# Optimization experiments

Measured on AMD Instinct MI355X. Metric: run time of the kernel, lower is better.

## Reference

```python
import jax, jax.numpy as jnp
import numpy as np

HIDDEN = 1024
FFN = 2816
N_EXPERTS = 8
TOP_K = 2
EPS = 1e-5
B, S = 2, 2048


def setup_inputs() -> dict:
    key = jax.random.key(0)
    ks = jax.random.split(key, 5)
    scale = 0.02
    return {
        "hidden_states": jax.random.normal(ks[0], (B, S, HIDDEN), dtype=jnp.float32),
        "ln_weight": jnp.ones((HIDDEN,), dtype=jnp.float32),
        "router_w": jax.random.normal(ks[1], (HIDDEN, N_EXPERTS), dtype=jnp.float32) * scale,
        "w1": jax.random.normal(ks[2], (N_EXPERTS, HIDDEN, FFN), dtype=jnp.float32) * scale,
        "w3": jax.random.normal(ks[3], (N_EXPERTS, HIDDEN, FFN), dtype=jnp.float32) * scale,
        "w2": jax.random.normal(ks[4], (N_EXPERTS, FFN, HIDDEN), dtype=jnp.float32) * scale,
    }


def _rms_norm(x, weight, eps):
    # LlamaRMSNorm: fp32 variance, scale by weight
    var = jnp.mean(jnp.square(x), axis=-1, keepdims=True)
    return x * jax.lax.rsqrt(var + eps) * weight


def reference(hidden_states, ln_weight, router_w, w1, w3, w2):
    b, s, h = hidden_states.shape
    x = _rms_norm(hidden_states, ln_weight, EPS).reshape(b * s, h)  # [T,H]

    # TopKRouter: softmax over experts, keep top-k gate probs
    logits = x @ router_w                       # [T,E]
    probs = jax.nn.softmax(logits, axis=-1)     # [T,E]
    top_p, top_i = jax.lax.top_k(probs, TOP_K)  # [T,K]
    # sparse gate matrix [T,E]: prob where selected, else 0 (dispatch+combine weights)
    gates = jnp.sum(jax.nn.one_hot(top_i, N_EXPERTS, dtype=x.dtype) * top_p[..., None], axis=1)

    # Experts: gated MLP (SwiGLU) per expert; dense-dispatch reference form,
    # combine masks out non-routed (gate==0) contributions.
    h1 = jnp.einsum("td,edf->tef", x, w1)       # [T,E,F]
    h3 = jnp.einsum("td,edf->tef", x, w3)       # [T,E,F]
    act = jax.nn.silu(h1) * h3                  # [T,E,F]
    y = jnp.einsum("tef,efd->ted", act, w2)     # [T,E,H]

    out = jnp.einsum("te,ted->td", gates, y)    # combine: [T,H]
    return out.reshape(b, s, h)
```

## Files before the change

### kernel.cpp

```cpp
#include <hip/hip_runtime.h>
#include <cstdint>
#include <cstddef>

#define TOKS 4096
#define HID  1024
#define FFN  2816
#define NE   8
#define CAP  4096

using floatx4 = __attribute__((ext_vector_type(4))) float;
using bf16x8  = __attribute__((ext_vector_type(8))) short;

__device__ __forceinline__ unsigned short f2bf(float f) {
    union { float f; unsigned int u; } v; v.f = f;
    unsigned int r = v.u + 0x7FFFu + ((v.u >> 16) & 1u);
    return (unsigned short)(r >> 16);
}

#define GLOAD16(g, l) __builtin_amdgcn_global_load_lds( \
    (__attribute__((address_space(1))) void*)(g),        \
    (__attribute__((address_space(3))) void*)(l), 16, 0, 0)

__global__ __launch_bounds__(256) void k_rmsnorm(const float* __restrict__ x,
                                                 const float* __restrict__ g,
                                                 unsigned short* __restrict__ xn)
{
    const int t = blockIdx.x;
    const int tid = threadIdx.x;
    const float4 v = *(const float4*)(x + (size_t)t*HID + tid*4);
    float ss = v.x*v.x + v.y*v.y + v.z*v.z + v.w*v.w;
    #pragma unroll
    for (int s = 32; s; s >>= 1) ss += __shfl_xor(ss, s, 64);
    __shared__ float red[4];
    if ((tid & 63) == 0) red[tid >> 6] = ss;
    __syncthreads();
    const float tot = red[0] + red[1] + red[2] + red[3];
    const float sc = rsqrtf(tot * (1.0f/HID) + 1e-5f);
    const float4 gw = *(const float4*)(g + tid*4);
    ushort4 o;
    o.x = f2bf(v.x*sc*gw.x); o.y = f2bf(v.y*sc*gw.y);
    o.z = f2bf(v.z*sc*gw.z); o.w = f2bf(v.w*sc*gw.w);
    *(ushort4*)(xn + (size_t)t*HID + tid*4) = o;
}

__global__ __launch_bounds__(256) void k_router(const float* __restrict__ x,
                                                const float* __restrict__ g,
                                                const float* __restrict__ rw,
                                                int* __restrict__ cnt,
                                                int* __restrict__ ids,
                                                float* __restrict__ gates)
{
    const int wid = threadIdx.x >> 6, lane = threadIdx.x & 63;
    const int t = blockIdx.x*4 + wid;
    const float* xr = x + (size_t)t*HID;
    float ss = 0.f;
    float acc[NE];
    #pragma unroll
    for (int e = 0; e < NE; ++e) acc[e] = 0.f;
    for (int h = lane; h < HID; h += 64) {
        const float xv = xr[h];
        ss += xv*xv;
        const float xg = xv * g[h];
        const float4 r0 = *(const float4*)(rw + h*NE);
        const float4 r1 = *(const float4*)(rw + h*NE + 4);
        acc[0] += xg*r0.x; acc[1] += xg*r0.y; acc[2] += xg*r0.z; acc[3] += xg*r0.w;
        acc[4] += xg*r1.x; acc[5] += xg*r1.y; acc[6] += xg*r1.z; acc[7] += xg*r1.w;
    }
    #pragma unroll
    for (int s = 32; s; s >>= 1) {
        ss += __shfl_xor(ss, s, 64);
        #pragma unroll
        for (int e = 0; e < NE; ++e) acc[e] += __shfl_xor(acc[e], s, 64);
    }
    if (lane == 0) {
        const float sc = rsqrtf(ss * (1.0f/HID) + 1e-5f);
        float p[NE];
        float m = -1e30f;
        #pragma unroll
        for (int e = 0; e < NE; ++e) { p[e] = acc[e]*sc; if (p[e] > m) m = p[e]; }
        float sum = 0.f;
        #pragma unroll
        for (int e = 0; e < NE; ++e) { p[e] = __expf(p[e] - m); sum += p[e]; }
        const float inv = 1.f / sum;
        int i1 = 0; float p1 = p[0];
        #pragma unroll
        for (int e = 1; e < NE; ++e) if (p[e] > p1) { p1 = p[e]; i1 = e; }
        int i2 = -1; float p2 = -1.f;
        #pragma unroll
        for (int e = 0; e < NE; ++e) if (e != i1 && p[e] > p2) { p2 = p[e]; i2 = e; }
        int s0 = atomicAdd(cnt + i1, 1);
        ids[i1*CAP + s0] = t; gates[i1*CAP + s0] = p1*inv;
        int s1 = atomicAdd(cnt + i2, 1);
        ids[i2*CAP + s1] = t; gates[i2*CAP + s1] = p2*inv;
    }
}

__global__ void k_scan(const int* __restrict__ cnt, int* __restrict__ off)
{
    if (threadIdx.x == 0) {
        int s = 0;
        for (int e = 0; e < NE; ++e) { off[e] = s; s += cnt[e]; }
        off[NE] = s;
    }
}

__global__ __launch_bounds__(256) void k_convtrans(const float* __restrict__ w1,
                                                   const float* __restrict__ w3,
                                                   const float* __restrict__ w2,
                                                   unsigned short* __restrict__ w1t,
                                                   unsigned short* __restrict__ w3t,
                                                   unsigned short* __restrict__ w2t)
{
    const int which = blockIdx.y;
    const int e = blockIdx.z;
    const float* src; unsigned short* dst; int R, C;
    if (which == 0)      { src = w1; dst = w1t; R = HID; C = FFN; }
    else if (which == 1) { src = w3; dst = w3t; R = HID; C = FFN; }
    else                 { src = w2; dst = w2t; R = FFN; C = HID; }
    src += (size_t)e * R * C;
    dst += (size_t)e * R * C;
    const int tiles_r = R >> 6;
    const int tr = blockIdx.x % tiles_r;
    const int tc = blockIdx.x / tiles_r;
    const int r0 = tr << 6, c0 = tc << 6;
    __shared__ unsigned short lds[64*66];
    const int tid = threadIdx.x;
    #pragma unroll
    for (int it = 0; it < 4; ++it) {
        const int id = it*256 + tid;
        const int r = id >> 4;
        const int c4 = (id & 15) << 2;
        const float4 v = *(const float4*)(src + (size_t)(r0 + r)*C + c0 + c4);
        lds[r*66 + c4 + 0] = f2bf(v.x);
        lds[r*66 + c4 + 1] = f2bf(v.y);
        lds[r*66 + c4 + 2] = f2bf(v.z);
        lds[r*66 + c4 + 3] = f2bf(v.w);
    }
    __syncthreads();
    #pragma unroll
    for (int it = 0; it < 2; ++it) {
        const int id = it*256 + tid;
        const int cc = id >> 3;
        const int rv = (id & 7) << 3;
        bf16x8 o;
        #pragma unroll
        for (int j = 0; j < 8; ++j) o[j] = (short)lds[(rv + j)*66 + cc];
        *(bf16x8*)(dst + (size_t)(c0 + cc)*R + r0 + rv) = o;
    }
}

__global__ __launch_bounds__(256, 4) void k_gemm1(
    const unsigned short* __restrict__ xn,
    const unsigned short* __restrict__ w1t,
    const unsigned short* __restrict__ w3t,
    const int* __restrict__ ids,
    const int* __restrict__ cnt,
    const int* __restrict__ off,
    unsigned short* __restrict__ act)
{
    const int e = blockIdx.z;
    const int cn = cnt[e];
    const int m0 = blockIdx.y * 128;
    if (m0 >= cn) return;
    const int n0 = blockIdx.x * 64;
    const int base = off[e];

    __shared__ __align__(16) unsigned short sA [128*64];
    __shared__ __align__(16) unsigned short sB1[64*64];
    __shared__ __align__(16) unsigned short sB3[64*64];

    const int tid  = threadIdx.x;
    const int wid  = tid >> 6;
    const int lane = tid & 63;
    const int lrow = lane >> 3;
    const int lchk = lane & 7;

    const unsigned short* aG[4];
    #pragma unroll
    for (int j = 0; j < 4; ++j) {
        const int row = (wid*4 + j)*8 + lrow;
        int rr = m0 + row; if (rr > cn - 1) rr = cn - 1;
        const int tok = ids[e*CAP + rr];
        const int c = lchk ^ (row & 7);
        aG[j] = xn + (size_t)tok*HID + c*8;
    }
    const unsigned short *b1G[2], *b3G[2];
    #pragma unroll
    for (int j = 0; j < 2; ++j) {
        const int row = (wid*2 + j)*8 + lrow;
        const int n = n0 + row;
        const int c = lchk ^ (row & 7);
        b1G[j] = w1t + ((size_t)e*FFN + n)*HID + c*8;
        b3G[j] = w3t + ((size_t)e*FFN + n)*HID + c*8;
    }

    floatx4 acc1[4][2], acc3[4][2];
    #pragma unroll
    for (int a = 0; a < 4; ++a)
      #pragma unroll
      for (int b = 0; b < 2; ++b) {
        acc1[a][b] = (floatx4){0.f,0.f,0.f,0.f};
        acc3[a][b] = (floatx4){0.f,0.f,0.f,0.f};
      }

    const int wm  = (wid >> 1) * 64;
    const int wn  = (wid & 1) * 32;
    const int r16 = lane & 15;
    const int q   = lane >> 4;
    const int rsw = r16 & 7;

    for (int kt = 0; kt < HID; kt += 64) {
        __syncthreads();
        #pragma unroll
        for (int j = 0; j < 4; ++j) GLOAD16(aG[j] + kt, sA + (wid*4 + j)*512);
        #pragma unroll
        for (int j = 0; j < 2; ++j) {
            GLOAD16(b1G[j] + kt, sB1 + (wid*2 + j)*512);
            GLOAD16(b3G[j] + kt, sB3 + (wid*2 + j)*512);
        }
        __syncthreads();
        #pragma unroll
        for (int kk = 0; kk < 2; ++kk) {
            const int slot = ((kk*4 + q) ^ rsw) << 3;
            bf16x8 a[4];
            #pragma unroll
            for (int mt = 0; mt < 4; ++mt)
                a[mt] = *(const bf16x8*)(sA + (wm + mt*16 + r16)*64 + slot);
            #pragma unroll
            for (int nt = 0; nt < 2; ++nt) {
                const bf16x8 b1 = *(const bf16x8*)(sB1 + (wn + nt*16 + r16)*64 + slot);
                const bf16x8 b3 = *(const bf16x8*)(sB3 + (wn + nt*16 + r16)*64 + slot);
                #pragma unroll
                for (int mt = 0; mt < 4; ++mt) {
                    acc1[mt][nt] = __builtin_amdgcn_mfma_f32_16x16x32_bf16(a[mt], b1, acc1[mt][nt], 0, 0, 0);
                    acc3[mt][nt] = __builtin_amdgcn_mfma_f32_16x16x32_bf16(a[mt], b3, acc3[mt][nt], 0, 0, 0);
                }
            }
        }
    }

    #pragma unroll
    for (int mt = 0; mt < 4; ++mt)
      #pragma unroll
      for (int i = 0; i < 4; ++i) {
        const int row = wm + mt*16 + q*4 + i;
        if (m0 + row < cn) {
            unsigned short* rp = act + (size_t)(base + m0 + row)*FFN + n0 + wn + r16;
            #pragma unroll
            for (int nt = 0; nt < 2; ++nt) {
                const float h1 = acc1[mt][nt][i];
                const float h3 = acc3[mt][nt][i];
                rp[nt*16] = f2bf(h1 / (1.f + __expf(-h1)) * h3);
            }
        }
      }
}

__global__ __launch_bounds__(256, 4) void k_gemm2(
    const unsigned short* __restrict__ act,
    const unsigned short* __restrict__ w2t,
    const int* __restrict__ ids,
    const float* __restrict__ gates,
    const int* __restrict__ cnt,
    const int* __restrict__ off,
    float* __restrict__ out)
{
    const int e = blockIdx.z;
    const int cn = cnt[e];
    const int m0 = blockIdx.y * 128;
    if (m0 >= cn) return;
    const int n0 = blockIdx.x * 64;
    const int base = off[e];

    __shared__ __align__(16) unsigned short sA[128*64];
    __shared__ __align__(16) unsigned short sB[64*64];

    const int tid  = threadIdx.x;
    const int wid  = tid >> 6;
    const int lane = tid & 63;
    const int lrow = lane >> 3;
    const int lchk = lane & 7;

    const unsigned short* aG[4];
    #pragma unroll
    for (int j = 0; j < 4; ++j) {
        const int row = (wid*4 + j)*8 + lrow;
        int rr = m0 + row; if (rr > cn - 1) rr = cn - 1;
        const int c = lchk ^ (row & 7);
        aG[j] = act + (size_t)(base + rr)*FFN + c*8;
    }
    const unsigned short* bG[2];
    #pragma unroll
    for (int j = 0; j < 2; ++j) {
        const int row = (wid*2 + j)*8 + lrow;
        const int c = lchk ^ (row & 7);
        bG[j] = w2t + ((size_t)e*HID + n0 + row)*FFN + c*8;
    }

    floatx4 acc[4][2];
    #pragma unroll
    for (int a = 0; a < 4; ++a)
      #pragma unroll
      for (int b = 0; b < 2; ++b) acc[a][b] = (floatx4){0.f,0.f,0.f,0.f};

    const int wm  = (wid >> 1) * 64;
    const int wn  = (wid & 1) * 32;
    const int r16 = lane & 15;
    const int q   = lane >> 4;
    const int rsw = r16 & 7;

    for (int kt = 0; kt < FFN; kt += 64) {
        __syncthreads();
        #pragma unroll
        for (int j = 0; j < 4; ++j) GLOAD16(aG[j] + kt, sA + (wid*4 + j)*512);
        #pragma unroll
        for (int j = 0; j < 2; ++j) GLOAD16(bG[j] + kt, sB + (wid*2 + j)*512);
        __syncthreads();
        #pragma unroll
        for (int kk = 0; kk < 2; ++kk) {
            const int slot = ((kk*4 + q) ^ rsw) << 3;
            bf16x8 a[4];
            #pragma unroll
            for (int mt = 0; mt < 4; ++mt)
                a[mt] = *(const bf16x8*)(sA + (wm + mt*16 + r16)*64 + slot);
            #pragma unroll
            for (int nt = 0; nt < 2; ++nt) {
                const bf16x8 b = *(const bf16x8*)(sB + (wn + nt*16 + r16)*64 + slot);
                #pragma unroll
                for (int mt = 0; mt < 4; ++mt)
                    acc[mt][nt] = __builtin_amdgcn_mfma_f32_16x16x32_bf16(a[mt], b, acc[mt][nt], 0, 0, 0);
            }
        }
    }

    #pragma unroll
    for (int mt = 0; mt < 4; ++mt)
      #pragma unroll
      for (int i = 0; i < 4; ++i) {
        const int row = wm + mt*16 + q*4 + i;
        if (m0 + row < cn) {
            const int idx = e*CAP + m0 + row;
            const int tok = ids[idx];
            const float gg = gates[idx];
            float* op = out + (size_t)tok*HID + n0 + wn + r16;
            #pragma unroll
            for (int nt = 0; nt < 2; ++nt)
                atomicAdd(op + nt*16, gg * acc[mt][nt][i]);
        }
      }
}

extern "C" void kernel_launch(void* const* d_in, const int* in_sizes, int n_in,
                              void* d_out, int out_size, void* d_ws, size_t ws_size,
                              hipStream_t stream)
{
    const float* hs  = (const float*)d_in[0];
    const float* lnw = (const float*)d_in[1];
    const float* rw  = (const float*)d_in[2];
    const float* w1  = (const float*)d_in[3];
    const float* w3  = (const float*)d_in[4];
    const float* w2  = (const float*)d_in[5];
    float* out = (float*)d_out;
    char* ws = (char*)d_ws;

    constexpr size_t WS_CNT   = 0;
    constexpr size_t WS_OFF   = 64;
    constexpr size_t WS_IDS   = 256;
    constexpr size_t WS_GATES = WS_IDS + sizeof(int)*NE*CAP;
    constexpr size_t WS_XN    = 327680;
    constexpr size_t WS_W1T   = WS_XN  + (size_t)2*TOKS*HID;
    constexpr size_t WS_W3T   = WS_W1T + (size_t)2*NE*FFN*HID;
    constexpr size_t WS_W2T   = WS_W3T + (size_t)2*NE*FFN*HID;
    constexpr size_t WS_ACT   = WS_W2T + (size_t)2*NE*FFN*HID;
    constexpr size_t WS_END   = WS_ACT + (size_t)2*2*TOKS*FFN;

    hipMemsetAsync(out, 0, sizeof(float)*(size_t)out_size, stream);
    if (ws_size < WS_END) return;
    hipMemsetAsync(ws, 0, 256, stream);

    int* cnt   = (int*)(ws + WS_CNT);
    int* off   = (int*)(ws + WS_OFF);
    int* ids   = (int*)(ws + WS_IDS);
    float* gts = (float*)(ws + WS_GATES);
    unsigned short* xn  = (unsigned short*)(ws + WS_XN);
    unsigned short* w1t = (unsigned short*)(ws + WS_W1T);
    unsigned short* w3t = (unsigned short*)(ws + WS_W3T);
    unsigned short* w2t = (unsigned short*)(ws + WS_W2T);
    unsigned short* act = (unsigned short*)(ws + WS_ACT);

    k_rmsnorm  <<<TOKS,            256, 0, stream>>>(hs, lnw, xn);
    k_router   <<<TOKS/4,          256, 0, stream>>>(hs, lnw, rw, cnt, ids, gts);
    k_scan     <<<1,               64,  0, stream>>>(cnt, off);
    k_convtrans<<<dim3(704,3,NE),  256, 0, stream>>>(w1, w3, w2, w1t, w3t, w2t);
    k_gemm1    <<<dim3(44,32,NE),  256, 0, stream>>>(xn, w1t, w3t, ids, cnt, off, act);
    k_gemm2    <<<dim3(16,32,NE),  256, 0, stream>>>(act, w2t, ids, gts, cnt, off, out);
}
```

Measured before the change: 756.8 us.

## Swap GEMM operand roles and replace atomic scatter with per-token combine kernel

Both expert GEMMs now put weights on the 128-row MFMA side and tokens on the 64-column side, so the weight tile is the larger one and output rows are written as vectorised ushort4/float4 stores. The second GEMM writes unweighted expert outputs to a temporary buffer (aliased onto the w1t workspace) instead of doing atomicAdd into the output. A new combine kernel reads each token's two slots, recorded by the router, and blends them with the gates, which also removes the output memset. The cost is an extra kernel and an extra round trip of expert outputs through memory, and correctness depends on w1t being dead by the time gemm2 reuses that space.

Measured after the change: 655.0 us. -13.5%, faster.

```diff
diff --git a/kernel.cpp b/kernel.cpp
--- a/kernel.cpp
+++ b/kernel.cpp
@@ -48,7 +48,8 @@
                                                 const float* __restrict__ rw,
                                                 int* __restrict__ cnt,
                                                 int* __restrict__ ids,
-                                                float* __restrict__ gates)
+                                                float* __restrict__ gates,
+                                                int* __restrict__ slot)
 {
     const int wid = threadIdx.x >> 6, lane = threadIdx.x & 63;
     const int t = blockIdx.x*4 + wid;
@@ -90,8 +91,10 @@
         for (int e = 0; e < NE; ++e) if (e != i1 && p[e] > p2) { p2 = p[e]; i2 = e; }
         int s0 = atomicAdd(cnt + i1, 1);
         ids[i1*CAP + s0] = t; gates[i1*CAP + s0] = p1*inv;
+        slot[t*2 + 0] = i1*CAP + s0;
         int s1 = atomicAdd(cnt + i2, 1);
         ids[i2*CAP + s1] = t; gates[i2*CAP + s1] = p2*inv;
+        slot[t*2 + 1] = i2*CAP + s1;
     }
 }
 
@@ -160,14 +163,14 @@
 {
     const int e = blockIdx.z;
     const int cn = cnt[e];
-    const int m0 = blockIdx.y * 128;
-    if (m0 >= cn) return;
-    const int n0 = blockIdx.x * 64;
+    const int t0 = blockIdx.y * 64;
+    if (t0 >= cn) return;
+    const int f0 = blockIdx.x * 128;
     const int base = off[e];
 
-    __shared__ __align__(16) unsigned short sA [128*64];
-    __shared__ __align__(16) unsigned short sB1[64*64];
-    __shared__ __align__(16) unsigned short sB3[64*64];
+    __shared__ __align__(16) unsigned short sA1[128*64];
+    __shared__ __align__(16) unsigned short sA3[128*64];
+    __shared__ __align__(16) unsigned short sB [64*64];
 
     const int tid  = threadIdx.x;
     const int wid  = tid >> 6;
@@ -175,23 +178,22 @@
     const int lrow = lane >> 3;
     const int lchk = lane & 7;
 
-    const unsigned short* aG[4];
+    const unsigned short *a1G[4], *a3G[4];
     #pragma unroll
     for (int j = 0; j < 4; ++j) {
         const int row = (wid*4 + j)*8 + lrow;
-        int rr = m0 + row; if (rr > cn - 1) rr = cn - 1;
+        const int c = lchk ^ (row & 7);
+        a1G[j] = w1t + ((size_t)e*FFN + f0 + row)*HID + c*8;
+        a3G[j] = w3t + ((size_t)e*FFN + f0 + row)*HID + c*8;
+    }
+    const unsigned short* bG[2];
+    #pragma unroll
+    for (int j = 0; j < 2; ++j) {
+        const int row = (wid*2 + j)*8 + lrow;
+        int rr = t0 + row; if (rr > cn - 1) rr = cn - 1;
         const int tok = ids[e*CAP + rr];
         const int c = lchk ^ (row & 7);
-        aG[j] = xn + (size_t)tok*HID + c*8;
-    }
-    const unsigned short *b1G[2], *b3G[2];
-    #pragma unroll
-    for (int j = 0; j < 2; ++j) {
-        const int row = (wid*2 + j)*8 + lrow;
-        const int n = n0 + row;
-        const int c = lchk ^ (row & 7);
-        b1G[j] = w1t + ((size_t)e*FFN + n)*HID + c*8;
-        b3G[j] = w3t + ((size_t)e*FFN + n)*HID + c*8;
+        bG[j] = xn + (size_t)tok*HID + c*8;
     }
 
     floatx4 acc1[4][2], acc3[4][2];
@@ -212,64 +214,65 @@
     for (int kt = 0; kt < HID; kt += 64) {
         __syncthreads();
         #pragma unroll
-        for (int j = 0; j < 4; ++j) GLOAD16(aG[j] + kt, sA + (wid*4 + j)*512);
-        #pragma unroll
-        for (int j = 0; j < 2; ++j) {
-            GLOAD16(b1G[j] + kt, sB1 + (wid*2 + j)*512);
-            GLOAD16(b3G[j] + kt, sB3 + (wid*2 + j)*512);
+        for (int j = 0; j < 4; ++j) {
+            GLOAD16(a1G[j] + kt, sA1 + (wid*4 + j)*512);
+            GLOAD16(a3G[j] + kt, sA3 + (wid*4 + j)*512);
         }
+        #pragma unroll
+        for (int j = 0; j < 2; ++j) GLOAD16(bG[j] + kt, sB + (wid*2 + j)*512);
         __syncthreads();
         #pragma unroll
         for (int kk = 0; kk < 2; ++kk) {
             const int slot = ((kk*4 + q) ^ rsw) << 3;
-            bf16x8 a[4];
-            #pragma unroll
-            for (int mt = 0; mt < 4; ++mt)
-                a[mt] = *(const bf16x8*)(sA + (wm + mt*16 + r16)*64 + slot);
+            bf16x8 a1[4], a3[4];
+            #pragma unroll
+            for (int mt = 0; mt < 4; ++mt) {
+                a1[mt] = *(const bf16x8*)(sA1 + (wm + mt*16 + r16)*64 + slot);
+                a3[mt] = *(const bf16x8*)(sA3 + (wm + mt*16 + r16)*64 + slot);
+            }
             #pragma unroll
             for (int nt = 0; nt < 2; ++nt) {
-                const bf16x8 b1 = *(const bf16x8*)(sB1 + (wn + nt*16 + r16)*64 + slot);
-                const bf16x8 b3 = *(const bf16x8*)(sB3 + (wn + nt*16 + r16)*64 + slot);
+                const bf16x8 b = *(const bf16x8*)(sB + (wn + nt*16 + r16)*64 + slot);
                 #pragma unroll
                 for (int mt = 0; mt < 4; ++mt) {
-                    acc1[mt][nt] = __builtin_amdgcn_mfma_f32_16x16x32_bf16(a[mt], b1, acc1[mt][nt], 0, 0, 0);
-                    acc3[mt][nt] = __builtin_amdgcn_mfma_f32_16x16x32_bf16(a[mt], b3, acc3[mt][nt], 0, 0, 0);
+                    acc1[mt][nt] = __builtin_amdgcn_mfma_f32_16x16x32_bf16(a1[mt], b, acc1[mt][nt], 0, 0, 0);
+                    acc3[mt][nt] = __builtin_amdgcn_mfma_f32_16x16x32_bf16(a3[mt], b, acc3[mt][nt], 0, 0, 0);
                 }
             }
         }
     }
 
     #pragma unroll
-    for (int mt = 0; mt < 4; ++mt)
-      #pragma unroll
-      for (int i = 0; i < 4; ++i) {
-        const int row = wm + mt*16 + q*4 + i;
-        if (m0 + row < cn) {
-            unsigned short* rp = act + (size_t)(base + m0 + row)*FFN + n0 + wn + r16;
-            #pragma unroll
-            for (int nt = 0; nt < 2; ++nt) {
-                const float h1 = acc1[mt][nt][i];
-                const float h3 = acc3[mt][nt][i];
-                rp[nt*16] = f2bf(h1 / (1.f + __expf(-h1)) * h3);
+    for (int nt = 0; nt < 2; ++nt) {
+        const int t = t0 + wn + nt*16 + r16;
+        if (t < cn) {
+            unsigned short* rp = act + (size_t)(base + t)*FFN + f0;
+            #pragma unroll
+            for (int mt = 0; mt < 4; ++mt) {
+                ushort4 o;
+                float h1, h3;
+                h1 = acc1[mt][nt][0]; h3 = acc3[mt][nt][0]; o.x = f2bf(h1/(1.f+__expf(-h1))*h3);
+                h1 = acc1[mt][nt][1]; h3 = acc3[mt][nt][1]; o.y = f2bf(h1/(1.f+__expf(-h1))*h3);
+                h1 = acc1[mt][nt][2]; h3 = acc3[mt][nt][2]; o.z = f2bf(h1/(1.f+__expf(-h1))*h3);
+                h1 = acc1[mt][nt][3]; h3 = acc3[mt][nt][3]; o.w = f2bf(h1/(1.f+__expf(-h1))*h3);
+                *(ushort4*)(rp + wm + mt*16 + q*4) = o;
             }
         }
-      }
+    }
 }
 
 __global__ __launch_bounds__(256, 4) void k_gemm2(
     const unsigned short* __restrict__ act,
     const unsigned short* __restrict__ w2t,
-    const int* __restrict__ ids,
-    const float* __restrict__ gates,
     const int* __restrict__ cnt,
     const int* __restrict__ off,
-    float* __restrict__ out)
+    float* __restrict__ ytmp)
 {
     const int e = blockIdx.z;
     const int cn = cnt[e];
-    const int m0 = blockIdx.y * 128;
-    if (m0 >= cn) return;
-    const int n0 = blockIdx.x * 64;
+    const int t0 = blockIdx.y * 64;
+    if (t0 >= cn) return;
+    const int h0 = blockIdx.x * 128;
     const int base = off[e];
 
     __shared__ __align__(16) unsigned short sA[128*64];
@@ -285,16 +288,16 @@
     #pragma unroll
     for (int j = 0; j < 4; ++j) {
         const int row = (wid*4 + j)*8 + lrow;
-        int rr = m0 + row; if (rr > cn - 1) rr = cn - 1;
         const int c = lchk ^ (row & 7);
-        aG[j] = act + (size_t)(base + rr)*FFN + c*8;
+        aG[j] = w2t + ((size_t)e*HID + h0 + row)*FFN + c*8;
     }
     const unsigned short* bG[2];
     #pragma unroll
     for (int j = 0; j < 2; ++j) {
         const int row = (wid*2 + j)*8 + lrow;
+        int rr = t0 + row; if (rr > cn - 1) rr = cn - 1;
         const int c = lchk ^ (row & 7);
-        bG[j] = w2t + ((size_t)e*HID + n0 + row)*FFN + c*8;
+        bG[j] = act + (size_t)(base + rr)*FFN + c*8;
     }
 
     floatx4 acc[4][2];
@@ -334,20 +337,39 @@
     }
 
     #pragma unroll
-    for (int mt = 0; mt < 4; ++mt)
-      #pragma unroll
-      for (int i = 0; i < 4; ++i) {
-        const int row = wm + mt*16 + q*4 + i;
-        if (m0 + row < cn) {
-            const int idx = e*CAP + m0 + row;
-            const int tok = ids[idx];
-            const float gg = gates[idx];
-            float* op = out + (size_t)tok*HID + n0 + wn + r16;
-            #pragma unroll
-            for (int nt = 0; nt < 2; ++nt)
-                atomicAdd(op + nt*16, gg * acc[mt][nt][i]);
+    for (int nt = 0; nt < 2; ++nt) {
+        const int t = t0 + wn + nt*16 + r16;
+        if (t < cn) {
+            float* rp = ytmp + (size_t)(base + t)*HID + h0;
+            #pragma unroll
+            for (int mt = 0; mt < 4; ++mt) {
+                float4 o = { acc[mt][nt][0], acc[mt][nt][1], acc[mt][nt][2], acc[mt][nt][3] };
+                *(float4*)(rp + wm + mt*16 + q*4) = o;
+            }
         }
-      }
+    }
+}
+
+__global__ __launch_bounds__(256) void k_combine(const float* __restrict__ ytmp,
+                                                 const int* __restrict__ slot,
+                                                 const float* __restrict__ gates,
+                                                 const int* __restrict__ off,
+                                                 float* __restrict__ out)
+{
+    const int t = blockIdx.x;
+    const int tid = threadIdx.x;
+    const int s0 = slot[t*2 + 0], s1 = slot[t*2 + 1];
+    const float g0 = gates[s0],    g1 = gates[s1];
+    const int c0 = off[s0 >> 12] + (s0 & (CAP-1));
+    const int c1 = off[s1 >> 12] + (s1 & (CAP-1));
+    const float4 y0 = *(const float4*)(ytmp + (size_t)c0*HID + tid*4);
+    const float4 y1 = *(const float4*)(ytmp + (size_t)c1*HID + tid*4);
+    float4 o;
+    o.x = g0*y0.x + g1*y1.x;
+    o.y = g0*y0.y + g1*y1.y;
+    o.z = g0*y0.z + g1*y1.z;
+    o.w = g0*y0.w + g1*y1.w;
+    *(float4*)(out + (size_t)t*HID + tid*4) = o;
 }
 
 extern "C" void kernel_launch(void* const* d_in, const int* in_sizes, int n_in,
@@ -367,6 +389,7 @@
     constexpr size_t WS_OFF   = 64;
     constexpr size_t WS_IDS   = 256;
     constexpr size_t WS_GATES = WS_IDS + sizeof(int)*NE*CAP;
+    constexpr size_t WS_SLOT  = WS_GATES + sizeof(float)*NE*CAP;
     constexpr size_t WS_XN    = 327680;
     constexpr size_t WS_W1T   = WS_XN  + (size_t)2*TOKS*HID;
     constexpr size_t WS_W3T   = WS_W1T + (size_t)2*NE*FFN*HID;
@@ -374,24 +397,26 @@
     constexpr size_t WS_ACT   = WS_W2T + (size_t)2*NE*FFN*HID;
     constexpr size_t WS_END   = WS_ACT + (size_t)2*2*TOKS*FFN;
 
-    hipMemsetAsync(out, 0, sizeof(float)*(size_t)out_size, stream);
-    if (ws_size < WS_END) return;
+    if (ws_size < WS_END) { hipMemsetAsync(out, 0, sizeof(float)*(size_t)out_size, stream); return; }
     hipMemsetAsync(ws, 0, 256, stream);
 
     int* cnt   = (int*)(ws + WS_CNT);
     int* off   = (int*)(ws + WS_OFF);
     int* ids   = (int*)(ws + WS_IDS);
     float* gts = (float*)(ws + WS_GATES);
+    int* slot  = (int*)(ws + WS_SLOT);
     unsigned short* xn  = (unsigned short*)(ws + WS_XN);
     unsigned short* w1t = (unsigned short*)(ws + WS_W1T);
     unsigned short* w3t = (unsigned short*)(ws + WS_W3T);
     unsigned short* w2t = (unsigned short*)(ws + WS_W2T);
     unsigned short* act = (unsigned short*)(ws + WS_ACT);
+    float* ytmp = (float*)(ws + WS_W1T);
 
     k_rmsnorm  <<<TOKS,            256, 0, stream>>>(hs, lnw, xn);
-    k_router   <<<TOKS/4,          256, 0, stream>>>(hs, lnw, rw, cnt, ids, gts);
+    k_router   <<<TOKS/4,          256, 0, stream>>>(hs, lnw, rw, cnt, ids, gts, slot);
     k_scan     <<<1,               64,  0, stream>>>(cnt, off);
     k_convtrans<<<dim3(704,3,NE),  256, 0, stream>>>(w1, w3, w2, w1t, w3t, w2t);
-    k_gemm1    <<<dim3(44,32,NE),  256, 0, stream>>>(xn, w1t, w3t, ids, cnt, off, act);
-    k_gemm2    <<<dim3(16,32,NE),  256, 0, stream>>>(act, w2t, ids, gts, cnt, off, out);
-}
+    k_gemm1    <<<dim3(22,64,NE),  256, 0, stream>>>(xn, w1t, w3t, ids, cnt, off, act);
+    k_gemm2    <<<dim3(8,64,NE),   256, 0, stream>>>(act, w2t, cnt, off, ytmp);
+    k_combine  <<<TOKS,            256, 0, stream>>>(ytmp, slot, gts, off, out);
+}
```
